# Optimization experiments

Hardware: AMD Instinct MI355X
Metric: run time of the kernel (lower is better)

## Reference

```python
import jax, jax.numpy as jnp
import numpy as np

INV_SCALE_SQ = 0.25  # module __init__ arg
N_SITES = 65536
SITE_DIM = 5  # (x, y, r, g, b)
H, W = 2048, 2048


def setup_inputs() -> dict:
    key = jax.random.key(0)
    k1, k2, k3, k4 = jax.random.split(key, 4)
    # site positions uniform over the image, colors uniform in [0,1]
    pos = jax.random.uniform(k1, (N_SITES, 2), dtype=jnp.float32) * jnp.array([W, H], jnp.float32)
    col = jax.random.uniform(k2, (N_SITES, 3), dtype=jnp.float32)
    sites = jnp.concatenate([pos, col], axis=-1)  # [N,5]
    cand0 = jax.random.randint(k3, (H, W), 0, N_SITES, dtype=jnp.int32)
    cand1 = jax.random.randint(k4, (H, W), 0, N_SITES, dtype=jnp.int32)
    return {"sites": sites, "cand0": cand0, "cand1": cand1, "width": W, "height": H}


def reference(sites, cand0, cand1, width, height):
    # per-pixel soft (anti-aliased) Voronoi rasterization of colored sites
    xs = jnp.arange(width, dtype=jnp.float32) + 0.5
    ys = jnp.arange(height, dtype=jnp.float32) + 0.5
    px = jnp.stack(jnp.meshgrid(xs, ys, indexing="xy"), axis=-1)  # [H,W,2] pixel centers
    s0 = sites[cand0]  # [H,W,5] gather candidate 0
    s1 = sites[cand1]  # [H,W,5] gather candidate 1
    d0 = jnp.sum((px - s0[..., :2]) ** 2, axis=-1)  # squared dist to site0
    d1 = jnp.sum((px - s1[..., :2]) ** 2, axis=-1)
    w = jax.nn.sigmoid((d1 - d0) * INV_SCALE_SQ)[..., None]  # weight toward closer site0
    out = w * s0[..., 2:] + (1.0 - w) * s1[..., 2:]  # [H,W,3]
    return out
```

## Files before the change

### kernel.cpp

```cpp
#include <hip/hip_runtime.h>


#define IMG_W 2048
#define IMG_H 2048
#define N_PIX (IMG_W * IMG_H)
#define INV_SCALE_SQ 0.25f

__global__ __launch_bounds__(256) void voronoi_soft_kernel(
    const float* __restrict__ sites,
    const int*   __restrict__ cand0,
    const int*   __restrict__ cand1,
    float*       __restrict__ out)
{
    const int tid = blockIdx.x * blockDim.x + threadIdx.x;
    const int pix = tid * 4;
    if (pix >= N_PIX) return;

    const int4 c0 = *reinterpret_cast<const int4*>(cand0 + pix);
    const int4 c1 = *reinterpret_cast<const int4*>(cand1 + pix);
    const int idx0[4] = {c0.x, c0.y, c0.z, c0.w};
    const int idx1[4] = {c1.x, c1.y, c1.z, c1.w};

    float res[12];

    const float py = (float)(pix >> 11) + 0.5f;
    const float px_base = (float)(pix & (IMG_W - 1)) + 0.5f;

#pragma unroll
    for (int i = 0; i < 4; ++i) {
        const float px = px_base + (float)i;
        const float* __restrict__ s0 = sites + (size_t)idx0[i] * 5;
        const float* __restrict__ s1 = sites + (size_t)idx1[i] * 5;

        const float s0x = s0[0], s0y = s0[1];
        const float s1x = s1[0], s1y = s1[1];

        const float dx0 = px - s0x, dy0 = py - s0y;
        const float dx1 = px - s1x, dy1 = py - s1y;
        const float d0 = dx0 * dx0 + dy0 * dy0;
        const float d1 = dx1 * dx1 + dy1 * dy1;

        const float t = (d1 - d0) * INV_SCALE_SQ;
        const float w = 1.0f / (1.0f + __expf(-t));
        const float wc = 1.0f - w;

        res[i * 3 + 0] = w * s0[2] + wc * s1[2];
        res[i * 3 + 1] = w * s0[3] + wc * s1[3];
        res[i * 3 + 2] = w * s0[4] + wc * s1[4];
    }

    float4* o = reinterpret_cast<float4*>(out + (size_t)pix * 3);
    o[0] = make_float4(res[0], res[1], res[2], res[3]);
    o[1] = make_float4(res[4], res[5], res[6], res[7]);
    o[2] = make_float4(res[8], res[9], res[10], res[11]);
}

extern "C" void kernel_launch(void* const* d_in, const int* in_sizes, int n_in,
                              void* d_out, int out_size, void* d_ws, size_t ws_size,
                              hipStream_t stream) {
    const float* sites = (const float*)d_in[0];
    const int*   cand0 = (const int*)d_in[1];
    const int*   cand1 = (const int*)d_in[2];
    float* out = (float*)d_out;

    const int threads = 256;
    const int pixels_per_thread = 4;
    const int total_threads = N_PIX / pixels_per_thread;
    const int blocks = total_threads / threads;

    voronoi_soft_kernel<<<blocks, threads, 0, stream>>>(sites, cand0, cand1, out);
}
```

Before: 161.2 us.

## Repack sites into 16-byte records with fp16 colors and use nontemporal streams

Adds a pre-pass that repacks each 5-float site into one 16-byte record: position in fp32, colors in fp16. The main kernel then fetches each candidate site with a single aligned 128-bit gather instead of five scattered scalar loads. The candidate index loads and the output stores are marked nontemporal to reduce cache pollution. This costs an extra small kernel launch and lowers color precision to fp16, which may exceed tolerance, and it keeps a fallback path for when workspace is too small.

```diff
diff --git a/kernel.cpp b/kernel.cpp
--- a/kernel.cpp
+++ b/kernel.cpp
@@ -1,12 +1,93 @@
 #include <hip/hip_runtime.h>
+#include <hip/hip_fp16.h>
 
 
 #define IMG_W 2048
 #define IMG_H 2048
 #define N_PIX (IMG_W * IMG_H)
+#define N_SITES 65536
 #define INV_SCALE_SQ 0.25f
 
+typedef int   vint4   __attribute__((ext_vector_type(4)));
+typedef float vfloat4 __attribute__((ext_vector_type(4)));
+
+__global__ __launch_bounds__(256) void repack_sites(
+    const float* __restrict__ sites, vfloat4* __restrict__ packed)
+{
+    const int i = blockIdx.x * blockDim.x + threadIdx.x;
+    const float* s = sites + (size_t)i * 5;
+    const __half2 rg = __floats2half2_rn(s[2], s[3]);
+    const __half2 b0 = __floats2half2_rn(s[4], 0.0f);
+    vfloat4 v;
+    v.x = s[0];
+    v.y = s[1];
+    v.z = __uint_as_float(*reinterpret_cast<const unsigned int*>(&rg));
+    v.w = __uint_as_float(*reinterpret_cast<const unsigned int*>(&b0));
+    packed[i] = v;
+}
+
+__device__ __forceinline__ float3 unpack_rgb(const vfloat4& rec) {
+    const unsigned int zu = __float_as_uint(rec.z);
+    const unsigned int wu = __float_as_uint(rec.w);
+    const __half2 rg = *reinterpret_cast<const __half2*>(&zu);
+    const __half2 b0 = *reinterpret_cast<const __half2*>(&wu);
+    const float2 rgf = __half22float2(rg);
+    return make_float3(rgf.x, rgf.y, __half2float(b0.x));
+}
+
 __global__ __launch_bounds__(256) void voronoi_soft_kernel(
+    const vfloat4* __restrict__ packed,
+    const int*     __restrict__ cand0,
+    const int*     __restrict__ cand1,
+    float*         __restrict__ out)
+{
+    const int tid = blockIdx.x * blockDim.x + threadIdx.x;
+    const int pix = tid * 4;
+
+    const vint4 c0 = __builtin_nontemporal_load(reinterpret_cast<const vint4*>(cand0 + pix));
+    const vint4 c1 = __builtin_nontemporal_load(reinterpret_cast<const vint4*>(cand1 + pix));
+    const int idx0[4] = {c0.x, c0.y, c0.z, c0.w};
+    const int idx1[4] = {c1.x, c1.y, c1.z, c1.w};
+
+    vfloat4 r0[4], r1[4];
+#pragma unroll
+    for (int i = 0; i < 4; ++i) r0[i] = packed[idx0[i]];
+#pragma unroll
+    for (int i = 0; i < 4; ++i) r1[i] = packed[idx1[i]];
+
+    const float py = (float)(pix >> 11) + 0.5f;
+    const float px_base = (float)(pix & (IMG_W - 1)) + 0.5f;
+
+    float res[12];
+#pragma unroll
+    for (int i = 0; i < 4; ++i) {
+        const float px = px_base + (float)i;
+        const float dx0 = px - r0[i].x, dy0 = py - r0[i].y;
+        const float dx1 = px - r1[i].x, dy1 = py - r1[i].y;
+        const float d0 = dx0 * dx0 + dy0 * dy0;
+        const float d1 = dx1 * dx1 + dy1 * dy1;
+
+        const float t = (d1 - d0) * INV_SCALE_SQ;
+        const float w = 1.0f / (1.0f + __expf(-t));
+        const float wc = 1.0f - w;
+
+        const float3 cA = unpack_rgb(r0[i]);
+        const float3 cB = unpack_rgb(r1[i]);
+        res[i * 3 + 0] = w * cA.x + wc * cB.x;
+        res[i * 3 + 1] = w * cA.y + wc * cB.y;
+        res[i * 3 + 2] = w * cA.z + wc * cB.z;
+    }
+
+    vfloat4* o = reinterpret_cast<vfloat4*>(out + (size_t)pix * 3);
+    vfloat4 o0 = {res[0], res[1], res[2], res[3]};
+    vfloat4 o1 = {res[4], res[5], res[6], res[7]};
+    vfloat4 o2 = {res[8], res[9], res[10], res[11]};
+    __builtin_nontemporal_store(o0, o + 0);
+    __builtin_nontemporal_store(o1, o + 1);
+    __builtin_nontemporal_store(o2, o + 2);
+}
+
+__global__ __launch_bounds__(256) void voronoi_soft_fallback(
     const float* __restrict__ sites,
     const int*   __restrict__ cand0,
     const int*   __restrict__ cand1,
@@ -14,41 +95,28 @@
 {
     const int tid = blockIdx.x * blockDim.x + threadIdx.x;
     const int pix = tid * 4;
-    if (pix >= N_PIX) return;
-
     const int4 c0 = *reinterpret_cast<const int4*>(cand0 + pix);
     const int4 c1 = *reinterpret_cast<const int4*>(cand1 + pix);
     const int idx0[4] = {c0.x, c0.y, c0.z, c0.w};
     const int idx1[4] = {c1.x, c1.y, c1.z, c1.w};
-
-    float res[12];
-
     const float py = (float)(pix >> 11) + 0.5f;
     const float px_base = (float)(pix & (IMG_W - 1)) + 0.5f;
-
+    float res[12];
 #pragma unroll
     for (int i = 0; i < 4; ++i) {
         const float px = px_base + (float)i;
-        const float* __restrict__ s0 = sites + (size_t)idx0[i] * 5;
-        const float* __restrict__ s1 = sites + (size_t)idx1[i] * 5;
-
-        const float s0x = s0[0], s0y = s0[1];
-        const float s1x = s1[0], s1y = s1[1];
-
-        const float dx0 = px - s0x, dy0 = py - s0y;
-        const float dx1 = px - s1x, dy1 = py - s1y;
+        const float* s0 = sites + (size_t)idx0[i] * 5;
+        const float* s1 = sites + (size_t)idx1[i] * 5;
+        const float dx0 = px - s0[0], dy0 = py - s0[1];
+        const float dx1 = px - s1[0], dy1 = py - s1[1];
         const float d0 = dx0 * dx0 + dy0 * dy0;
         const float d1 = dx1 * dx1 + dy1 * dy1;
-
-        const float t = (d1 - d0) * INV_SCALE_SQ;
-        const float w = 1.0f / (1.0f + __expf(-t));
+        const float w = 1.0f / (1.0f + __expf(-(d1 - d0) * INV_SCALE_SQ));
         const float wc = 1.0f - w;
-
         res[i * 3 + 0] = w * s0[2] + wc * s1[2];
         res[i * 3 + 1] = w * s0[3] + wc * s1[3];
         res[i * 3 + 2] = w * s0[4] + wc * s1[4];
     }
-
     float4* o = reinterpret_cast<float4*>(out + (size_t)pix * 3);
     o[0] = make_float4(res[0], res[1], res[2], res[3]);
     o[1] = make_float4(res[4], res[5], res[6], res[7]);
@@ -64,9 +132,14 @@
     float* out = (float*)d_out;
 
     const int threads = 256;
-    const int pixels_per_thread = 4;
-    const int total_threads = N_PIX / pixels_per_thread;
-    const int blocks = total_threads / threads;
+    const int blocks = N_PIX / (4 * threads);
 
-    voronoi_soft_kernel<<<blocks, threads, 0, stream>>>(sites, cand0, cand1, out);
+    const size_t packed_bytes = (size_t)N_SITES * sizeof(vfloat4);
+    if (ws_size >= packed_bytes) {
+        vfloat4* packed = (vfloat4*)d_ws;
+        repack_sites<<<N_SITES / 256, 256, 0, stream>>>(sites, packed);
+        voronoi_soft_kernel<<<blocks, threads, 0, stream>>>(packed, cand0, cand1, out);
+    } else {
+        voronoi_soft_fallback<<<blocks, threads, 0, stream>>>(sites, cand0, cand1, out);
+    }
 }
```

New measurement: 138.5 us. 1.16x faster.
